# Kernel optimization log

Measured on AMD Instinct MI355X. Metric: run time of the kernel, lower is better.

The kernel has to match this reference:

```python
import jax, jax.numpy as jnp
import numpy as np
from jax import lax

B, C, H, W = 32, 64, 56, 56
G = 4            # num_heads*2 with num_heads=2
SMK, K = 5, 7
C2 = C // 2
HEAD_DIM = C // G
SCALE = HEAD_DIM ** -0.5


def _bias_idx(k, h, w):
    # static replica of ContMix.generate_idx + apply_rpb index construction
    rpb_size = 2 * k - 1
    idx_h = np.arange(k)
    idx_w = np.arange(k)
    idx_k = (idx_h[:, None] * rpb_size + idx_w).reshape(-1)
    rep_h = np.ones(k, np.int64); rep_h[k // 2] = h - (k - 1)
    rep_w = np.ones(k, np.int64); rep_w[k // 2] = w - (k - 1)
    bias_hw = np.repeat(idx_h, rep_h)[:, None] * rpb_size + np.repeat(idx_w, rep_w)  # (h, w)
    bias_idx = (bias_hw[..., None] + idx_k).reshape(-1, k * k)[::-1]  # torch.flip dim 0
    return jnp.asarray(bias_idx.copy())

IDX1 = _bias_idx(SMK, H, W)
IDX2 = _bias_idx(K, H, W)


def setup_inputs() -> dict:
    key = jax.random.key(0)
    ks = jax.random.split(key, 18)
    r = lambda i, sh: jax.random.normal(ks[i], sh, jnp.float32)
    return dict(
        x=r(0, (B, C, H, W)),
        lepe_w=r(1, (C, 1, K, K)) * 0.1,
        lepe_b=r(2, (C,)) * 0.1,
        lepe_bn_s=1.0 + 0.1 * r(3, (C,)),
        lepe_bn_b=0.1 * r(4, (C,)),
        wq_w=r(5, (C2, C2)) * (C2 ** -0.5),
        wq_bn_s=1.0 + 0.1 * r(6, (C2,)),
        wq_bn_b=0.1 * r(7, (C2,)),
        wk_w=r(8, (C2, C2)) * (C2 ** -0.5),
        wk_bn_s=1.0 + 0.1 * r(9, (C2,)),
        wk_bn_b=0.1 * r(10, (C2,)),
        wp_w=r(11, (SMK * SMK + K * K, 49)) * (49 ** -0.5),
        wp_b=0.1 * r(12, (SMK * SMK + K * K,)),
        rpb1=0.02 * r(13, (G, 2 * SMK - 1, 2 * SMK - 1)),
        rpb2=0.02 * r(14, (G, 2 * K - 1, 2 * K - 1)),
        dy_w=r(15, (C, C)) * (C ** -0.5),
        dy_bn_s=1.0 + 0.1 * r(16, (C,)),
        dy_bn_b=0.1 * r(17, (C,)),
    )


def _per_ch(t):
    return t[None, :, None, None]


def _contmix(x, lepe_w, lepe_b, lepe_bn_s, lepe_bn_b, wq_w, wq_bn_s, wq_bn_b,
             wk_w, wk_bn_s, wk_bn_b, wp_w, wp_b, rpb1, rpb2, dy_w, dy_bn_s, dy_bn_b):
    # lepe: deploy-mode DilatedReparamBlock = depthwise 7x7 conv (+bias), then eval BN
    lepe = lax.conv_general_dilated(x, lepe_w, (1, 1), [(K // 2, K // 2)] * 2,
                                    feature_group_count=C)
    lepe = (lepe + _per_ch(lepe_b)) * _per_ch(lepe_bn_s) + _per_ch(lepe_bn_b)

    q, kf = jnp.split(x, 2, axis=1)                         # (B, C2, H, W) each
    q = jnp.einsum('oi,bihw->bohw', wq_w, q)                # weight_query 1x1 conv
    q = (q * _per_ch(wq_bn_s) + _per_ch(wq_bn_b)) * SCALE
    # weight_key: AdaptiveAvgPool2d(7) -> 1x1 conv -> BN (H,W divisible by 7)
    kp = kf.reshape(B, C2, 7, H // 7, 7, W // 7).mean(axis=(3, 5))
    kp = jnp.einsum('oi,bihw->bohw', wk_w, kp)
    kp = kp * _per_ch(wk_bn_s) + _per_ch(wk_bn_b)

    qg = q.reshape(B, G, C2 // G, H * W)                    # b g c n
    kg = kp.reshape(B, G, C2 // G, 49)                      # b g c l
    w = jnp.einsum('bgcn,bgcl->bgnl', qg, kg)               # (B, G, HW, 49)
    # weight_proj: 1x1 conv over the 49 pooled-context channels
    w = jnp.einsum('ml,bgnl->bgnm', wp_w, w) + wp_b         # (B, G, HW, 74)
    w = w.reshape(B, G, H, W, SMK * SMK + K * K)

    attn1 = w[..., :SMK * SMK]
    attn2 = w[..., SMK * SMK:]
    attn1 = attn1 + rpb1.reshape(G, -1)[:, IDX1].reshape(1, G, H, W, SMK * SMK)
    attn2 = attn2 + rpb2.reshape(G, -1)[:, IDX2].reshape(1, G, H, W, K * K)
    attn1 = jax.nn.softmax(attn1, axis=-1)
    attn2 = jax.nn.softmax(attn2, axis=-1)

    c = C // (2 * G)                                        # value head dim = 8
    v = x.reshape(B, 2, G, c, H, W)                         # 'b (m g c) h w'

    def dyn_mix(attn, val, k):
        # unfold + einsum: content-adaptive depthwise mixing
        p = lax.conv_general_dilated_patches(
            val.reshape(B, G * c, H, W), (k, k), (1, 1), [(k // 2, k // 2)] * 2,
            dimension_numbers=('NCHW', 'OIHW', 'NCHW'))
        p = p.reshape(B, G, c, k * k, H, W)                 # channel-major patch layout
        return jnp.einsum('bgckhw,bghwk->bgchw', p, attn)

    x1 = dyn_mix(attn1, v[:, 0], SMK)
    x2 = dyn_mix(attn2, v[:, 1], K)
    out = jnp.concatenate([x1, x2], axis=1).reshape(B, C, H, W)
    out = jnp.einsum('oi,bihw->bohw', dy_w, out)            # dyconv_proj 1x1 + BN
    out = out * _per_ch(dy_bn_s) + _per_ch(dy_bn_b)
    return out + lepe


def reference(x, lepe_w, lepe_b, lepe_bn_s, lepe_bn_b, wq_w, wq_bn_s, wq_bn_b,
              wk_w, wk_bn_s, wk_bn_b, wp_w, wp_b, rpb1, rpb2, dy_w, dy_bn_s, dy_bn_b):
    return _contmix(x, lepe_w, lepe_b, lepe_bn_s, lepe_bn_b, wq_w, wq_bn_s, wq_bn_b,
                    wk_w, wk_bn_s, wk_bn_b, wp_w, wp_b, rpb1, rpb2, dy_w, dy_bn_s, dy_bn_b)
```

## Files before the change

kernel.cpp:

```cpp
#include <hip/hip_runtime.h>

#define BB 32
#define CC 64
#define HH 56
#define WW 56
#define HW 3136
#define TW 64
#define TR 12

__global__ __launch_bounds__(256) void pool_k(const float* __restrict__ x,
                                              float* __restrict__ pws) {
    const int py = blockIdx.x;
    const int b  = blockIdx.y;
    const int tid = threadIdx.x;
    if (tid >= 224) return;
    const int i = tid / 7, px = tid % 7;
    const float4* xp4 = reinterpret_cast<const float4*>(
        x + ((long)(b * CC + 32 + i)) * HW + py * 8 * WW + px * 8);
    float4 sA = make_float4(0.f, 0.f, 0.f, 0.f);
    float4 sB = make_float4(0.f, 0.f, 0.f, 0.f);
    #pragma unroll
    for (int y = 0; y < 8; ++y) {
        const float4 a = xp4[y * 14];
        const float4 c = xp4[y * 14 + 1];
        sA.x += a.x; sA.y += a.y; sA.z += a.z; sA.w += a.w;
        sB.x += c.x; sB.y += c.y; sB.z += c.z; sB.w += c.w;
    }
    pws[(long)b * 1568 + i * 49 + py * 7 + px] =
        (sA.x + sA.y + sA.z + sA.w + sB.x + sB.y + sB.z + sB.w) * (1.f / 64.f);
}

__global__ __launch_bounds__(256) void wk_k(const float* __restrict__ pws,
                                            const float* __restrict__ wk,
                                            const float* __restrict__ wks,
                                            const float* __restrict__ wkb,
                                            const float* __restrict__ wp_w,
                                            float* __restrict__ WK) {
    __shared__ float p_s[32 * 49];
    __shared__ float kg_s[8 * 49];
    const int b = blockIdx.x >> 2;
    const int g = blockIdx.x & 3;
    const int tid = threadIdx.x;
    for (int idx = tid; idx < 1568; idx += 256) p_s[idx] = pws[(long)b * 1568 + idx];
    __syncthreads();
    for (int idx = tid; idx < 392; idx += 256) {
        const int o8 = idx / 49, l = idx % 49;
        const int o = g * 8 + o8;
        float acc = 0.f;
        #pragma unroll
        for (int i = 0; i < 32; ++i) acc = fmaf(wk[o * 32 + i], p_s[i * 49 + l], acc);
        kg_s[idx] = acc * wks[o] + wkb[o];
    }
    __syncthreads();
    for (int idx = tid; idx < 640; idx += 256) {
        const int c = idx / 80, slot = idx % 80;
        float acc = 0.f;
        int m = -1;
        if (slot < 28) { if (slot < 25) m = slot; }
        else           { if (slot < 77) m = 25 + (slot - 28); }
        if (m >= 0) {
            const float* kp = kg_s + c * 49;
            #pragma unroll
            for (int l = 0; l < 49; ++l) acc = fmaf(wp_w[m * 49 + l], kp[l], acc);
        }
        const long base = (long)blockIdx.x * 640;
        if (slot < 28) WK[base + c * 28 + slot] = acc;
        else           WK[base + 224 + c * 52 + (slot - 28)] = acc;
    }
}

__global__ __launch_bounds__(256) void attnmix_k(const float* __restrict__ x,
                                                 const float* __restrict__ WK,
                                                 const float* __restrict__ wq_w,
                                                 const float* __restrict__ wq_s,
                                                 const float* __restrict__ wq_bb,
                                                 const float* __restrict__ wp_b,
                                                 const float* __restrict__ rpb1,
                                                 const float* __restrict__ rpb2,
                                                 const float* __restrict__ lw,
                                                 const float* __restrict__ lb,
                                                 const float* __restrict__ ls,
                                                 const float* __restrict__ lbb,
                                                 float* __restrict__ mix,
                                                 float* __restrict__ out) {
    __shared__ __align__(16) float tile[8 * TR * TW];
    __shared__ __align__(16) float WK1_s[8 * 28];
    __shared__ __align__(16) float WK2_s[8 * 52];
    __shared__ __align__(16) float wqT_s[32 * 8];
    __shared__ __align__(16) float wpb1_s[28];
    __shared__ __align__(16) float wpb2_s[52];
    __shared__ __align__(16) float lw_s[8 * 56];
    __shared__ float rpb1_s[81];
    __shared__ float rpb2_s[169];
    __shared__ float wqbn_s[16];
    __shared__ float lbn_s[48];
    const int tid = threadIdx.x;
    const int bg = blockIdx.y;
    const int g = bg & 3, b = bg >> 2;

    {
        const float* wkp = WK + (long)bg * 640;
        for (int i = tid; i < 224; i += 256) WK1_s[i] = wkp[i];
        for (int i = tid; i < 416; i += 256) WK2_s[i] = wkp[224 + i];
    }
    {
        const int i = tid >> 3, c = tid & 7;
        wqT_s[tid] = wq_w[(g * 8 + c) * 32 + i];
    }
    if (tid < 28) wpb1_s[tid] = (tid < 25) ? wp_b[tid] : 0.f;
    if (tid >= 32 && tid < 84) wpb2_s[tid - 32] = (tid < 81) ? wp_b[25 + tid - 32] : 0.f;
    if (tid < 81) rpb1_s[tid] = rpb1[g * 81 + tid];
    if (tid < 169) rpb2_s[tid] = rpb2[g * 169 + tid];
    if (tid >= 192 && tid < 200) wqbn_s[tid - 192] = wq_s[g * 8 + tid - 192];
    if (tid >= 200 && tid < 208) wqbn_s[8 + tid - 200] = wq_bb[g * 8 + tid - 200];
    for (int i = tid; i < 448; i += 256) {
        const int ch = i / 56, rem = i % 56, row = rem >> 3, j = rem & 7;
        lw_s[i] = (j < 7) ? lw[(g * 8 + ch) * 49 + row * 7 + j] : 0.f;
    }
    if (tid < 16) {
        const int c = (tid < 8) ? (g * 8 + tid) : (32 + g * 8 + tid - 8);
        lbn_s[tid] = lb[c]; lbn_s[16 + tid] = ls[c]; lbn_s[32 + tid] = lbb[c];
    }

    const int N0 = blockIdx.x << 8;
    const int ph0 = N0 / WW;
    const int r0 = ph0 - 3;

    {
        const float* xc = x + ((long)b * CC + g * 8) * HW;
        #pragma unroll
        for (int ch = 0; ch < 8; ++ch)
            for (int k = tid; k < TR * TW; k += 256) {
                const int row = k >> 6, lxx = k & 63;
                const int gy = r0 + row, gx = lxx - 3;
                float v = 0.f;
                if ((unsigned)gy < HH && (unsigned)gx < WW) v = xc[ch * HW + gy * WW + gx];
                tile[ch * (TR * TW) + k] = v;
            }
    }
    __syncthreads();

    const int n = N0 + tid;
    const bool valid = n < HW;
    const int nc = valid ? n : HW - 1;
    const int ph = nc / WW, pw = nc % WW;
    const int yr = HH - 1 - ph, xr = WW - 1 - pw;
    const int lrow = ph - r0;
    const int tb0 = (lrow - 3) * TW + pw;

    const float* xb = x + (long)b * CC * HW + nc;

    float q8[8];
    #pragma unroll
    for (int c = 0; c < 8; ++c) q8[c] = 0.f;
    for (int i = 0; i < 32; ++i) {
        const float xv = xb[i * HW];
        const float4 wA = *reinterpret_cast<const float4*>(wqT_s + i * 8);
        const float4 wB = *reinterpret_cast<const float4*>(wqT_s + i * 8 + 4);
        q8[0] = fmaf(wA.x, xv, q8[0]); q8[1] = fmaf(wA.y, xv, q8[1]);
        q8[2] = fmaf(wA.z, xv, q8[2]); q8[3] = fmaf(wA.w, xv, q8[3]);
        q8[4] = fmaf(wB.x, xv, q8[4]); q8[5] = fmaf(wB.y, xv, q8[5]);
        q8[6] = fmaf(wB.z, xv, q8[6]); q8[7] = fmaf(wB.w, xv, q8[7]);
    }
    #pragma unroll
    for (int c = 0; c < 8; ++c)
        q8[c] = (q8[c] * wqbn_s[c] + wqbn_s[8 + c]) * 0.25f;

    __builtin_amdgcn_sched_barrier(0);

    {
        float w1[25];
        {
            const float4* wp4 = reinterpret_cast<const float4*>(wpb1_s);
            #pragma unroll
            for (int qd = 0; qd < 6; ++qd) {
                const float4 bv = wp4[qd];
                w1[qd * 4 + 0] = bv.x; w1[qd * 4 + 1] = bv.y;
                w1[qd * 4 + 2] = bv.z; w1[qd * 4 + 3] = bv.w;
            }
            w1[24] = wpb1_s[24];
        }
        #pragma unroll
        for (int c = 0; c < 8; ++c) {
            const float qv = q8[c];
            const float4* kr = reinterpret_cast<const float4*>(WK1_s + c * 28);
            #pragma unroll
            for (int qd = 0; qd < 6; ++qd) {
                const float4 kv = kr[qd];
                w1[qd * 4 + 0] = fmaf(qv, kv.x, w1[qd * 4 + 0]);
                w1[qd * 4 + 1] = fmaf(qv, kv.y, w1[qd * 4 + 1]);
                w1[qd * 4 + 2] = fmaf(qv, kv.z, w1[qd * 4 + 2]);
                w1[qd * 4 + 3] = fmaf(qv, kv.w, w1[qd * 4 + 3]);
            }
            w1[24] = fmaf(qv, WK1_s[c * 28 + 24], w1[24]);
        }
        const int rh5 = yr < 2 ? yr : (yr > 53 ? yr - 51 : 2);
        const int rw5 = xr < 2 ? xr : (xr > 53 ? xr - 51 : 2);
        #pragma unroll
        for (int i = 0; i < 5; ++i)
            #pragma unroll
            for (int j = 0; j < 5; ++j)
                w1[i * 5 + j] += rpb1_s[(rh5 + i) * 9 + (rw5 + j)];
        float mx = -1e30f;
        #pragma unroll
        for (int m = 0; m < 25; ++m) mx = fmaxf(mx, w1[m]);
        float sm = 0.f;
        #pragma unroll
        for (int m = 0; m < 25; ++m) { w1[m] = __expf(w1[m] - mx); sm += w1[m]; }
        const float r = 1.f / sm;
        #pragma unroll
        for (int m = 0; m < 25; ++m) w1[m] *= r;

        float* m0 = mix + ((long)b * CC + g * 8) * HW + nc;
        float* o0 = out + ((long)b * CC + g * 8) * HW + nc;
        #pragma unroll
        for (int ch = 0; ch < 8; ++ch) {
            const float* t = tile + ch * (TR * TW) + tb0;
            const float* lwc = lw_s + ch * 56;
            float a = 0.f, la = 0.f;
            #pragma unroll
            for (int i = 0; i < 7; ++i) {
                const float4 lA = *reinterpret_cast<const float4*>(lwc + i * 8);
                const float4 lB = *reinterpret_cast<const float4*>(lwc + i * 8 + 4);
                const float lwv[7] = {lA.x, lA.y, lA.z, lA.w, lB.x, lB.y, lB.z};
                #pragma unroll
                for (int j = 0; j < 7; ++j) {
                    const float v = t[i * TW + j];
                    la = fmaf(lwv[j], v, la);
                    if (i >= 1 && i <= 5 && j >= 1 && j <= 5)
                        a = fmaf(w1[(i - 1) * 5 + (j - 1)], v, a);
                }
            }
            if (valid) {
                m0[ch * HW] = a;
                o0[ch * HW] = (la + lbn_s[ch]) * lbn_s[16 + ch] + lbn_s[32 + ch];
            }
        }
    }

    __syncthreads();
    {
        const float* xc = x + ((long)b * CC + 32 + g * 8) * HW;
        #pragma unroll
        for (int ch = 0; ch < 8; ++ch)
            for (int k = tid; k < TR * TW; k += 256) {
                const int row = k >> 6, lxx = k & 63;
                const int gy = r0 + row, gx = lxx - 3;
                float v = 0.f;
                if ((unsigned)gy < HH && (unsigned)gx < WW) v = xc[ch * HW + gy * WW + gx];
                tile[ch * (TR * TW) + k] = v;
            }
        for (int i = tid; i < 448; i += 256) {
            const int ch = i / 56, rem = i % 56, row = rem >> 3, j = rem & 7;
            lw_s[i] = (j < 7) ? lw[(32 + g * 8 + ch) * 49 + row * 7 + j] : 0.f;
        }
    }
    __syncthreads();

    {
        float w2[49];
        {
            const float4* wp4 = reinterpret_cast<const float4*>(wpb2_s);
            #pragma unroll
            for (int qd = 0; qd < 12; ++qd) {
                const float4 bv = wp4[qd];
                w2[qd * 4 + 0] = bv.x; w2[qd * 4 + 1] = bv.y;
                w2[qd * 4 + 2] = bv.z; w2[qd * 4 + 3] = bv.w;
            }
            w2[48] = wpb2_s[48];
        }
        #pragma unroll
        for (int c = 0; c < 8; ++c) {
            const float qv = q8[c];
            const float4* kr = reinterpret_cast<const float4*>(WK2_s + c * 52);
            #pragma unroll
            for (int qd = 0; qd < 12; ++qd) {
                const float4 kv = kr[qd];
                w2[qd * 4 + 0] = fmaf(qv, kv.x, w2[qd * 4 + 0]);
                w2[qd * 4 + 1] = fmaf(qv, kv.y, w2[qd * 4 + 1]);
                w2[qd * 4 + 2] = fmaf(qv, kv.z, w2[qd * 4 + 2]);
                w2[qd * 4 + 3] = fmaf(qv, kv.w, w2[qd * 4 + 3]);
            }
            w2[48] = fmaf(qv, WK2_s[c * 52 + 48], w2[48]);
        }
        const int rh7 = yr < 3 ? yr : (yr > 52 ? yr - 49 : 3);
        const int rw7 = xr < 3 ? xr : (xr > 52 ? xr - 49 : 3);
        #pragma unroll
        for (int i = 0; i < 7; ++i)
            #pragma unroll
            for (int j = 0; j < 7; ++j)
                w2[i * 7 + j] += rpb2_s[(rh7 + i) * 13 + (rw7 + j)];
        float mx = -1e30f;
        #pragma unroll
        for (int m = 0; m < 49; ++m) mx = fmaxf(mx, w2[m]);
        float sm = 0.f;
        #pragma unroll
        for (int m = 0; m < 49; ++m) { w2[m] = __expf(w2[m] - mx); sm += w2[m]; }
        const float r = 1.f / sm;
        #pragma unroll
        for (int m = 0; m < 49; ++m) w2[m] *= r;

        float* m1 = mix + ((long)b * CC + 32 + g * 8) * HW + nc;
        float* o1 = out + ((long)b * CC + 32 + g * 8) * HW + nc;
        #pragma unroll
        for (int ch = 0; ch < 8; ++ch) {
            const float* t = tile + ch * (TR * TW) + tb0;
            const float* lwc = lw_s + ch * 56;
            float a = 0.f, la = 0.f;
            #pragma unroll
            for (int i = 0; i < 7; ++i) {
                const float4 lA = *reinterpret_cast<const float4*>(lwc + i * 8);
                const float4 lB = *reinterpret_cast<const float4*>(lwc + i * 8 + 4);
                const float lwv[7] = {lA.x, lA.y, lA.z, lA.w, lB.x, lB.y, lB.z};
                #pragma unroll
                for (int j = 0; j < 7; ++j) {
                    const float v = t[i * TW + j];
                    la = fmaf(lwv[j], v, la);
                    a  = fmaf(w2[i * 7 + j], v, a);
                }
            }
            if (valid) {
                m1[ch * HW] = a;
                o1[ch * HW] = (la + lbn_s[8 + ch]) * lbn_s[16 + 8 + ch] + lbn_s[32 + 8 + ch];
            }
        }
    }
}

__global__ __launch_bounds__(256) void final_k(const float* __restrict__ mix,
                                               const float* __restrict__ dy_w,
                                               const float* __restrict__ s,
                                               const float* __restrict__ bb,
                                               float* __restrict__ out) {
    __shared__ float w_s[64 * 64];
    const int tid = threadIdx.x;
    const int b = blockIdx.y;
    for (int i = tid; i < 4096; i += 256) w_s[(i & 63) * 64 + (i >> 6)] = dy_w[i];
    __syncthreads();
    const int oo = (tid >> 5) * 8;
    const int p4 = blockIdx.x * 32 + (tid & 31);
    if (p4 >= 784) return;
    const float* mp = mix + (long)b * CC * HW + p4 * 4;
    float4 acc[8];
    #pragma unroll
    for (int o = 0; o < 8; ++o) acc[o] = make_float4(0.f, 0.f, 0.f, 0.f);
    for (int ii = 0; ii < 64; ii += 8) {
        float4 mv[8];
        #pragma unroll
        for (int u = 0; u < 8; ++u)
            mv[u] = *reinterpret_cast<const float4*>(mp + (long)(ii + u) * HW);
        #pragma unroll
        for (int u = 0; u < 8; ++u) {
            const float* wr = w_s + (ii + u) * 64 + oo;
            #pragma unroll
            for (int o = 0; o < 8; ++o) {
                const float wv = wr[o];
                acc[o].x = fmaf(wv, mv[u].x, acc[o].x);
                acc[o].y = fmaf(wv, mv[u].y, acc[o].y);
                acc[o].z = fmaf(wv, mv[u].z, acc[o].z);
                acc[o].w = fmaf(wv, mv[u].w, acc[o].w);
            }
        }
    }
    float* op = out + (long)b * CC * HW + p4 * 4;
    #pragma unroll
    for (int o = 0; o < 8; ++o) {
        const float sc = s[oo + o], bc = bb[oo + o];
        float4* dst = reinterpret_cast<float4*>(op + (long)(oo + o) * HW);
        float4 prev = *dst;
        prev.x = fmaf(acc[o].x, sc, bc) + prev.x;
        prev.y = fmaf(acc[o].y, sc, bc) + prev.y;
        prev.z = fmaf(acc[o].z, sc, bc) + prev.z;
        prev.w = fmaf(acc[o].w, sc, bc) + prev.w;
        *dst = prev;
    }
}

extern "C" void kernel_launch(void* const* d_in, const int* in_sizes, int n_in,
                              void* d_out, int out_size, void* d_ws, size_t ws_size,
                              hipStream_t stream) {
    const float* x       = (const float*)d_in[0];
    const float* lepe_w  = (const float*)d_in[1];
    const float* lepe_b  = (const float*)d_in[2];
    const float* lepe_s  = (const float*)d_in[3];
    const float* lepe_bb = (const float*)d_in[4];
    const float* wq_w    = (const float*)d_in[5];
    const float* wq_s    = (const float*)d_in[6];
    const float* wq_bb   = (const float*)d_in[7];
    const float* wk_w    = (const float*)d_in[8];
    const float* wk_s    = (const float*)d_in[9];
    const float* wk_bb   = (const float*)d_in[10];
    const float* wp_w    = (const float*)d_in[11];
    const float* wp_b    = (const float*)d_in[12];
    const float* rpb1    = (const float*)d_in[13];
    const float* rpb2    = (const float*)d_in[14];
    const float* dy_w    = (const float*)d_in[15];
    const float* dy_s    = (const float*)d_in[16];
    const float* dy_bb   = (const float*)d_in[17];
    float* out = (float*)d_out;

    float* ws     = (float*)d_ws;
    float* WK_ws  = ws;
    float* mix_ws = WK_ws + 128 * 640;
    float* p_ws   = mix_ws + 32 * 64 * HW;

    const int nTiles = (HW + 255) / 256;

    pool_k<<<dim3(7, BB), 256, 0, stream>>>(x, p_ws);
    wk_k<<<dim3(BB * 4), 256, 0, stream>>>(p_ws, wk_w, wk_s, wk_bb, wp_w, WK_ws);
    attnmix_k<<<dim3(nTiles, BB * 4), 256, 0, stream>>>(x, WK_ws, wq_w, wq_s, wq_bb,
                                                        wp_b, rpb1, rpb2,
                                                        lepe_w, lepe_b, lepe_s, lepe_bb,
                                                        mix_ws, out);
    final_k<<<dim3(25, BB), 256, 0, stream>>>(mix_ws, dy_w, dy_s, dy_bb, out);
}
```

Baseline: 250.3 us.

## Precompute q in separate pass and split attention kernel into two branch kernels

Moves the per-pixel q projection (32→32 1x1 conv with BN and scale) out of the attention kernel into a batched pass that shares a launch with the WK computation, writing q to a workspace buffer. Splits the fused attnmix kernel into attn1 (5x5 branch) and attn2 (7x7 branch), giving each smaller register and shared-memory footprints and twice as many blocks. This is meant to cut the redundant q recompute across the two branches and improve occupancy, at the cost of an extra q write/read through global memory, one more kernel launch, and reloading the x tile in each kernel.

```diff
diff --git a/kernel.cpp b/kernel.cpp
--- a/kernel.cpp
+++ b/kernel.cpp
@@ -30,17 +30,75 @@
         (sA.x + sA.y + sA.z + sA.w + sB.x + sB.y + sB.z + sB.w) * (1.f / 64.f);
 }
 
-__global__ __launch_bounds__(256) void wk_k(const float* __restrict__ pws,
-                                            const float* __restrict__ wk,
-                                            const float* __restrict__ wks,
-                                            const float* __restrict__ wkb,
-                                            const float* __restrict__ wp_w,
-                                            float* __restrict__ WK) {
+__global__ __launch_bounds__(256) void qwk_k(const float* __restrict__ x,
+                                             const float* __restrict__ pws,
+                                             const float* __restrict__ wk,
+                                             const float* __restrict__ wks,
+                                             const float* __restrict__ wkb,
+                                             const float* __restrict__ wp_w,
+                                             const float* __restrict__ wq_w,
+                                             const float* __restrict__ wq_s,
+                                             const float* __restrict__ wq_bb,
+                                             float* __restrict__ WK,
+                                             float* __restrict__ qws) {
     __shared__ float p_s[32 * 49];
     __shared__ float kg_s[8 * 49];
-    const int b = blockIdx.x >> 2;
-    const int g = blockIdx.x & 3;
+    __shared__ float wqT_s[32 * 32];
+    __shared__ float qbn_s[64];
     const int tid = threadIdx.x;
+    const int bx = blockIdx.x;
+
+    if (bx < 800) {
+        for (int idx = tid; idx < 1024; idx += 256) {
+            const int o = idx & 31, i = idx >> 5;
+            wqT_s[i * 32 + o] = wq_w[o * 32 + i];
+        }
+        if (tid < 32) { qbn_s[tid] = wq_s[tid]; qbn_s[32 + tid] = wq_bb[tid]; }
+        __syncthreads();
+        const int b = bx / 25, t = bx % 25;
+        const int p4 = t * 32 + (tid & 31);
+        if (p4 >= 784) return;
+        const int oo = (tid >> 5) * 4;
+        const float* xp = x + (long)b * CC * HW + p4 * 4;
+        float4 acc[4];
+        #pragma unroll
+        for (int o = 0; o < 4; ++o) acc[o] = make_float4(0.f, 0.f, 0.f, 0.f);
+        for (int ii = 0; ii < 32; ii += 8) {
+            float4 mv[8];
+            #pragma unroll
+            for (int u = 0; u < 8; ++u)
+                mv[u] = *reinterpret_cast<const float4*>(xp + (long)(ii + u) * HW);
+            #pragma unroll
+            for (int u = 0; u < 8; ++u) {
+                const float* wr = wqT_s + (ii + u) * 32 + oo;
+                #pragma unroll
+                for (int o = 0; o < 4; ++o) {
+                    const float wv = wr[o];
+                    acc[o].x = fmaf(wv, mv[u].x, acc[o].x);
+                    acc[o].y = fmaf(wv, mv[u].y, acc[o].y);
+                    acc[o].z = fmaf(wv, mv[u].z, acc[o].z);
+                    acc[o].w = fmaf(wv, mv[u].w, acc[o].w);
+                }
+            }
+        }
+        float* qp = qws + (long)b * 32 * HW + p4 * 4;
+        #pragma unroll
+        for (int o = 0; o < 4; ++o) {
+            const float sc = qbn_s[oo + o] * 0.25f;
+            const float bc = qbn_s[32 + oo + o] * 0.25f;
+            float4 r;
+            r.x = fmaf(acc[o].x, sc, bc);
+            r.y = fmaf(acc[o].y, sc, bc);
+            r.z = fmaf(acc[o].z, sc, bc);
+            r.w = fmaf(acc[o].w, sc, bc);
+            *reinterpret_cast<float4*>(qp + (long)(oo + o) * HW) = r;
+        }
+        return;
+    }
+
+    const int id = bx - 800;
+    const int b = id >> 2;
+    const int g = id & 3;
     for (int idx = tid; idx < 1568; idx += 256) p_s[idx] = pws[(long)b * 1568 + idx];
     __syncthreads();
     for (int idx = tid; idx < 392; idx += 256) {
@@ -63,71 +121,68 @@
             #pragma unroll
             for (int l = 0; l < 49; ++l) acc = fmaf(wp_w[m * 49 + l], kp[l], acc);
         }
-        const long base = (long)blockIdx.x * 640;
+        const long base = (long)id * 640;
         if (slot < 28) WK[base + c * 28 + slot] = acc;
         else           WK[base + 224 + c * 52 + (slot - 28)] = acc;
     }
 }
 
-__global__ __launch_bounds__(256) void attnmix_k(const float* __restrict__ x,
-                                                 const float* __restrict__ WK,
-                                                 const float* __restrict__ wq_w,
-                                                 const float* __restrict__ wq_s,
-                                                 const float* __restrict__ wq_bb,
-                                                 const float* __restrict__ wp_b,
-                                                 const float* __restrict__ rpb1,
-                                                 const float* __restrict__ rpb2,
-                                                 const float* __restrict__ lw,
-                                                 const float* __restrict__ lb,
-                                                 const float* __restrict__ ls,
-                                                 const float* __restrict__ lbb,
-                                                 float* __restrict__ mix,
-                                                 float* __restrict__ out) {
+__global__ __launch_bounds__(256) void attn1_k(const float* __restrict__ x,
+                                               const float* __restrict__ WK,
+                                               const float* __restrict__ qws,
+                                               const float* __restrict__ wp_b,
+                                               const float* __restrict__ rpb1,
+                                               const float* __restrict__ lw,
+                                               const float* __restrict__ lb,
+                                               const float* __restrict__ ls,
+                                               const float* __restrict__ lbb,
+                                               float* __restrict__ mix,
+                                               float* __restrict__ out) {
     __shared__ __align__(16) float tile[8 * TR * TW];
     __shared__ __align__(16) float WK1_s[8 * 28];
-    __shared__ __align__(16) float WK2_s[8 * 52];
-    __shared__ __align__(16) float wqT_s[32 * 8];
     __shared__ __align__(16) float wpb1_s[28];
-    __shared__ __align__(16) float wpb2_s[52];
     __shared__ __align__(16) float lw_s[8 * 56];
     __shared__ float rpb1_s[81];
-    __shared__ float rpb2_s[169];
-    __shared__ float wqbn_s[16];
-    __shared__ float lbn_s[48];
+    __shared__ float lbn_s[24];
     const int tid = threadIdx.x;
     const int bg = blockIdx.y;
     const int g = bg & 3, b = bg >> 2;
+    const int ch0 = g * 8;
 
     {
         const float* wkp = WK + (long)bg * 640;
-        for (int i = tid; i < 224; i += 256) WK1_s[i] = wkp[i];
-        for (int i = tid; i < 416; i += 256) WK2_s[i] = wkp[224 + i];
-    }
-    {
-        const int i = tid >> 3, c = tid & 7;
-        wqT_s[tid] = wq_w[(g * 8 + c) * 32 + i];
+        if (tid < 224) WK1_s[tid] = wkp[tid];
     }
     if (tid < 28) wpb1_s[tid] = (tid < 25) ? wp_b[tid] : 0.f;
-    if (tid >= 32 && tid < 84) wpb2_s[tid - 32] = (tid < 81) ? wp_b[25 + tid - 32] : 0.f;
     if (tid < 81) rpb1_s[tid] = rpb1[g * 81 + tid];
-    if (tid < 169) rpb2_s[tid] = rpb2[g * 169 + tid];
-    if (tid >= 192 && tid < 200) wqbn_s[tid - 192] = wq_s[g * 8 + tid - 192];
-    if (tid >= 200 && tid < 208) wqbn_s[8 + tid - 200] = wq_bb[g * 8 + tid - 200];
     for (int i = tid; i < 448; i += 256) {
         const int ch = i / 56, rem = i % 56, row = rem >> 3, j = rem & 7;
-        lw_s[i] = (j < 7) ? lw[(g * 8 + ch) * 49 + row * 7 + j] : 0.f;
-    }
-    if (tid < 16) {
-        const int c = (tid < 8) ? (g * 8 + tid) : (32 + g * 8 + tid - 8);
-        lbn_s[tid] = lb[c]; lbn_s[16 + tid] = ls[c]; lbn_s[32 + tid] = lbb[c];
+        lw_s[i] = (j < 7) ? lw[(ch0 + ch) * 49 + row * 7 + j] : 0.f;
+    }
+    if (tid >= 232 && tid < 240) {
+        const int c = ch0 + tid - 232;
+        lbn_s[tid - 232] = lb[c]; lbn_s[8 + tid - 232] = ls[c]; lbn_s[16 + tid - 232] = lbb[c];
     }
 
     const int N0 = blockIdx.x << 8;
     const int ph0 = N0 / WW;
     const int r0 = ph0 - 3;
 
-    {
-        const float* xc = x + ((long)b * CC + g * 8) * HW;
+    const int n = N0 + tid;
+    const bool valid = n < HW;
+    const int nc = valid ? n : HW - 1;
+    const int ph = nc / WW, pw = nc % WW;
+    const int yr = HH - 1 - ph, xr = WW - 1 - pw;
+    const int lrow = ph - r0;
+    const int tb0 = (lrow - 3) * TW + pw;
+
+    const float* qp = qws + ((long)b * 32 + ch0) * HW + nc;
+    float q8[8];
+    #pragma unroll
+    for (int c = 0; c < 8; ++c) q8[c] = qp[c * HW];
+
+    {
+        const float* xc = x + ((long)b * CC + ch0) * HW;
         #pragma unroll
         for (int ch = 0; ch < 8; ++ch)
             for (int k = tid; k < TR * TW; k += 256) {
@@ -140,6 +195,116 @@
     }
     __syncthreads();
 
+    float w1[25];
+    {
+        const float4* wp4 = reinterpret_cast<const float4*>(wpb1_s);
+        #pragma unroll
+        for (int qd = 0; qd < 6; ++qd) {
+            const float4 bv = wp4[qd];
+            w1[qd * 4 + 0] = bv.x; w1[qd * 4 + 1] = bv.y;
+            w1[qd * 4 + 2] = bv.z; w1[qd * 4 + 3] = bv.w;
+        }
+        w1[24] = wpb1_s[24];
+    }
+    #pragma unroll
+    for (int c = 0; c < 8; ++c) {
+        const float qv = q8[c];
+        const float4* kr = reinterpret_cast<const float4*>(WK1_s + c * 28);
+        #pragma unroll
+        for (int qd = 0; qd < 6; ++qd) {
+            const float4 kv = kr[qd];
+            w1[qd * 4 + 0] = fmaf(qv, kv.x, w1[qd * 4 + 0]);
+            w1[qd * 4 + 1] = fmaf(qv, kv.y, w1[qd * 4 + 1]);
+            w1[qd * 4 + 2] = fmaf(qv, kv.z, w1[qd * 4 + 2]);
+            w1[qd * 4 + 3] = fmaf(qv, kv.w, w1[qd * 4 + 3]);
+        }
+        w1[24] = fmaf(qv, WK1_s[c * 28 + 24], w1[24]);
+    }
+    const int rh5 = yr < 2 ? yr : (yr > 53 ? yr - 51 : 2);
+    const int rw5 = xr < 2 ? xr : (xr > 53 ? xr - 51 : 2);
+    #pragma unroll
+    for (int i = 0; i < 5; ++i)
+        #pragma unroll
+        for (int j = 0; j < 5; ++j)
+            w1[i * 5 + j] += rpb1_s[(rh5 + i) * 9 + (rw5 + j)];
+    float mx = -1e30f;
+    #pragma unroll
+    for (int m = 0; m < 25; ++m) mx = fmaxf(mx, w1[m]);
+    float sm = 0.f;
+    #pragma unroll
+    for (int m = 0; m < 25; ++m) { w1[m] = __expf(w1[m] - mx); sm += w1[m]; }
+    const float r = 1.f / sm;
+    #pragma unroll
+    for (int m = 0; m < 25; ++m) w1[m] *= r;
+
+    float* m0 = mix + ((long)b * CC + ch0) * HW + nc;
+    float* o0 = out + ((long)b * CC + ch0) * HW + nc;
+    #pragma unroll
+    for (int ch = 0; ch < 8; ++ch) {
+        const float* t = tile + ch * (TR * TW) + tb0;
+        const float* lwc = lw_s + ch * 56;
+        float a = 0.f, la = 0.f;
+        #pragma unroll
+        for (int i = 0; i < 7; ++i) {
+            const float4 lA = *reinterpret_cast<const float4*>(lwc + i * 8);
+            const float4 lB = *reinterpret_cast<const float4*>(lwc + i * 8 + 4);
+            const float lwv[7] = {lA.x, lA.y, lA.z, lA.w, lB.x, lB.y, lB.z};
+            #pragma unroll
+            for (int j = 0; j < 7; ++j) {
+                const float v = t[i * TW + j];
+                la = fmaf(lwv[j], v, la);
+                if (i >= 1 && i <= 5 && j >= 1 && j <= 5)
+                    a = fmaf(w1[(i - 1) * 5 + (j - 1)], v, a);
+            }
+        }
+        if (valid) {
+            m0[ch * HW] = a;
+            o0[ch * HW] = (la + lbn_s[ch]) * lbn_s[8 + ch] + lbn_s[16 + ch];
+        }
+    }
+}
+
+__global__ __launch_bounds__(256) void attn2_k(const float* __restrict__ x,
+                                               const float* __restrict__ WK,
+                                               const float* __restrict__ qws,
+                                               const float* __restrict__ wp_b,
+                                               const float* __restrict__ rpb2,
+                                               const float* __restrict__ lw,
+                                               const float* __restrict__ lb,
+                                               const float* __restrict__ ls,
+                                               const float* __restrict__ lbb,
+                                               float* __restrict__ mix,
+                                               float* __restrict__ out) {
+    __shared__ __align__(16) float tile[8 * TR * TW];
+    __shared__ __align__(16) float WK2_s[8 * 52];
+    __shared__ __align__(16) float wpb2_s[52];
+    __shared__ __align__(16) float lw_s[8 * 56];
+    __shared__ float rpb2_s[169];
+    __shared__ float lbn_s[24];
+    const int tid = threadIdx.x;
+    const int bg = blockIdx.y;
+    const int g = bg & 3, b = bg >> 2;
+    const int ch0 = 32 + g * 8;
+
+    {
+        const float* wkp = WK + (long)bg * 640 + 224;
+        for (int i = tid; i < 416; i += 256) WK2_s[i] = wkp[i];
+    }
+    if (tid < 52) wpb2_s[tid] = (tid < 49) ? wp_b[25 + tid] : 0.f;
+    if (tid >= 64 && tid < 233) rpb2_s[tid - 64] = rpb2[g * 169 + (tid - 64)];
+    for (int i = tid; i < 448; i += 256) {
+        const int ch = i / 56, rem = i % 56, row = rem >> 3, j = rem & 7;
+        lw_s[i] = (j < 7) ? lw[(ch0 + ch) * 49 + row * 7 + j] : 0.f;
+    }
+    if (tid >= 240 && tid < 248) {
+        const int c = ch0 + tid - 240;
+        lbn_s[tid - 240] = lb[c]; lbn_s[8 + tid - 240] = ls[c]; lbn_s[16 + tid - 240] = lbb[c];
+    }
+
+    const int N0 = blockIdx.x << 8;
+    const int ph0 = N0 / WW;
+    const int r0 = ph0 - 3;
+
     const int n = N0 + tid;
     const bool valid = n < HW;
     const int nc = valid ? n : HW - 1;
@@ -148,99 +313,13 @@
     const int lrow = ph - r0;
     const int tb0 = (lrow - 3) * TW + pw;
 
-    const float* xb = x + (long)b * CC * HW + nc;
-
+    const float* qp = qws + ((long)b * 32 + g * 8) * HW + nc;
     float q8[8];
     #pragma unroll
-    for (int c = 0; c < 8; ++c) q8[c] = 0.f;
-    for (int i = 0; i < 32; ++i) {
-        const float xv = xb[i * HW];
-        const float4 wA = *reinterpret_cast<const float4*>(wqT_s + i * 8);
-        const float4 wB = *reinterpret_cast<const float4*>(wqT_s + i * 8 + 4);
-        q8[0] = fmaf(wA.x, xv, q8[0]); q8[1] = fmaf(wA.y, xv, q8[1]);
-        q8[2] = fmaf(wA.z, xv, q8[2]); q8[3] = fmaf(wA.w, xv, q8[3]);
-        q8[4] = fmaf(wB.x, xv, q8[4]); q8[5] = fmaf(wB.y, xv, q8[5]);
-        q8[6] = fmaf(wB.z, xv, q8[6]); q8[7] = fmaf(wB.w, xv, q8[7]);
-    }
-    #pragma unroll
-    for (int c = 0; c < 8; ++c)
-        q8[c] = (q8[c] * wqbn_s[c] + wqbn_s[8 + c]) * 0.25f;
-
-    __builtin_amdgcn_sched_barrier(0);
-
-    {
-        float w1[25];
-        {
-            const float4* wp4 = reinterpret_cast<const float4*>(wpb1_s);
-            #pragma unroll
-            for (int qd = 0; qd < 6; ++qd) {
-                const float4 bv = wp4[qd];
-                w1[qd * 4 + 0] = bv.x; w1[qd * 4 + 1] = bv.y;
-                w1[qd * 4 + 2] = bv.z; w1[qd * 4 + 3] = bv.w;
-            }
-            w1[24] = wpb1_s[24];
-        }
-        #pragma unroll
-        for (int c = 0; c < 8; ++c) {
-            const float qv = q8[c];
-            const float4* kr = reinterpret_cast<const float4*>(WK1_s + c * 28);
-            #pragma unroll
-            for (int qd = 0; qd < 6; ++qd) {
-                const float4 kv = kr[qd];
-                w1[qd * 4 + 0] = fmaf(qv, kv.x, w1[qd * 4 + 0]);
-                w1[qd * 4 + 1] = fmaf(qv, kv.y, w1[qd * 4 + 1]);
-                w1[qd * 4 + 2] = fmaf(qv, kv.z, w1[qd * 4 + 2]);
-                w1[qd * 4 + 3] = fmaf(qv, kv.w, w1[qd * 4 + 3]);
-            }
-            w1[24] = fmaf(qv, WK1_s[c * 28 + 24], w1[24]);
-        }
-        const int rh5 = yr < 2 ? yr : (yr > 53 ? yr - 51 : 2);
-        const int rw5 = xr < 2 ? xr : (xr > 53 ? xr - 51 : 2);
-        #pragma unroll
-        for (int i = 0; i < 5; ++i)
-            #pragma unroll
-            for (int j = 0; j < 5; ++j)
-                w1[i * 5 + j] += rpb1_s[(rh5 + i) * 9 + (rw5 + j)];
-        float mx = -1e30f;
-        #pragma unroll
-        for (int m = 0; m < 25; ++m) mx = fmaxf(mx, w1[m]);
-        float sm = 0.f;
-        #pragma unroll
-        for (int m = 0; m < 25; ++m) { w1[m] = __expf(w1[m] - mx); sm += w1[m]; }
-        const float r = 1.f / sm;
-        #pragma unroll
-        for (int m = 0; m < 25; ++m) w1[m] *= r;
-
-        float* m0 = mix + ((long)b * CC + g * 8) * HW + nc;
-        float* o0 = out + ((long)b * CC + g * 8) * HW + nc;
-        #pragma unroll
-        for (int ch = 0; ch < 8; ++ch) {
-            const float* t = tile + ch * (TR * TW) + tb0;
-            const float* lwc = lw_s + ch * 56;
-            float a = 0.f, la = 0.f;
-            #pragma unroll
-            for (int i = 0; i < 7; ++i) {
-                const float4 lA = *reinterpret_cast<const float4*>(lwc + i * 8);
-                const float4 lB = *reinterpret_cast<const float4*>(lwc + i * 8 + 4);
-                const float lwv[7] = {lA.x, lA.y, lA.z, lA.w, lB.x, lB.y, lB.z};
-                #pragma unroll
-                for (int j = 0; j < 7; ++j) {
-                    const float v = t[i * TW + j];
-                    la = fmaf(lwv[j], v, la);
-                    if (i >= 1 && i <= 5 && j >= 1 && j <= 5)
-                        a = fmaf(w1[(i - 1) * 5 + (j - 1)], v, a);
-                }
-            }
-            if (valid) {
-                m0[ch * HW] = a;
-                o0[ch * HW] = (la + lbn_s[ch]) * lbn_s[16 + ch] + lbn_s[32 + ch];
-            }
-        }
-    }
-
-    __syncthreads();
-    {
-        const float* xc = x + ((long)b * CC + 32 + g * 8) * HW;
+    for (int c = 0; c < 8; ++c) q8[c] = qp[c * HW];
+
+    {
+        const float* xc = x + ((long)b * CC + ch0) * HW;
         #pragma unroll
         for (int ch = 0; ch < 8; ++ch)
             for (int k = tid; k < TR * TW; k += 256) {
@@ -250,79 +329,73 @@
                 if ((unsigned)gy < HH && (unsigned)gx < WW) v = xc[ch * HW + gy * WW + gx];
                 tile[ch * (TR * TW) + k] = v;
             }
-        for (int i = tid; i < 448; i += 256) {
-            const int ch = i / 56, rem = i % 56, row = rem >> 3, j = rem & 7;
-            lw_s[i] = (j < 7) ? lw[(32 + g * 8 + ch) * 49 + row * 7 + j] : 0.f;
-        }
     }
     __syncthreads();
 
-    {
-        float w2[49];
-        {
-            const float4* wp4 = reinterpret_cast<const float4*>(wpb2_s);
-            #pragma unroll
-            for (int qd = 0; qd < 12; ++qd) {
-                const float4 bv = wp4[qd];
-                w2[qd * 4 + 0] = bv.x; w2[qd * 4 + 1] = bv.y;
-                w2[qd * 4 + 2] = bv.z; w2[qd * 4 + 3] = bv.w;
-            }
-            w2[48] = wpb2_s[48];
-        }
-        #pragma unroll
-        for (int c = 0; c < 8; ++c) {
-            const float qv = q8[c];
-            const float4* kr = reinterpret_cast<const float4*>(WK2_s + c * 52);
-            #pragma unroll
-            for (int qd = 0; qd < 12; ++qd) {
-                const float4 kv = kr[qd];
-                w2[qd * 4 + 0] = fmaf(qv, kv.x, w2[qd * 4 + 0]);
-                w2[qd * 4 + 1] = fmaf(qv, kv.y, w2[qd * 4 + 1]);
-                w2[qd * 4 + 2] = fmaf(qv, kv.z, w2[qd * 4 + 2]);
-                w2[qd * 4 + 3] = fmaf(qv, kv.w, w2[qd * 4 + 3]);
-            }
-            w2[48] = fmaf(qv, WK2_s[c * 52 + 48], w2[48]);
-        }
-        const int rh7 = yr < 3 ? yr : (yr > 52 ? yr - 49 : 3);
-        const int rw7 = xr < 3 ? xr : (xr > 52 ? xr - 49 : 3);
-        #pragma unroll
-        for (int i = 0; i < 7; ++i)
-            #pragma unroll
-            for (int j = 0; j < 7; ++j)
-                w2[i * 7 + j] += rpb2_s[(rh7 + i) * 13 + (rw7 + j)];
-        float mx = -1e30f;
-        #pragma unroll
-        for (int m = 0; m < 49; ++m) mx = fmaxf(mx, w2[m]);
-        float sm = 0.f;
-        #pragma unroll
-        for (int m = 0; m < 49; ++m) { w2[m] = __expf(w2[m] - mx); sm += w2[m]; }
-        const float r = 1.f / sm;
-        #pragma unroll
-        for (int m = 0; m < 49; ++m) w2[m] *= r;
-
-        float* m1 = mix + ((long)b * CC + 32 + g * 8) * HW + nc;
-        float* o1 = out + ((long)b * CC + 32 + g * 8) * HW + nc;
-        #pragma unroll
-        for (int ch = 0; ch < 8; ++ch) {
-            const float* t = tile + ch * (TR * TW) + tb0;
-            const float* lwc = lw_s + ch * 56;
-            float a = 0.f, la = 0.f;
-            #pragma unroll
-            for (int i = 0; i < 7; ++i) {
-                const float4 lA = *reinterpret_cast<const float4*>(lwc + i * 8);
-                const float4 lB = *reinterpret_cast<const float4*>(lwc + i * 8 + 4);
-                const float lwv[7] = {lA.x, lA.y, lA.z, lA.w, lB.x, lB.y, lB.z};
-                #pragma unroll
-                for (int j = 0; j < 7; ++j) {
-                    const float v = t[i * TW + j];
-                    la = fmaf(lwv[j], v, la);
-                    a  = fmaf(w2[i * 7 + j], v, a);
-                }
-            }
-            if (valid) {
-                m1[ch * HW] = a;
-                o1[ch * HW] = (la + lbn_s[8 + ch]) * lbn_s[16 + 8 + ch] + lbn_s[32 + 8 + ch];
-            }
+    float w2[49];
+    {
+        const float4* wp4 = reinterpret_cast<const float4*>(wpb2_s);
+        #pragma unroll
+        for (int qd = 0; qd < 12; ++qd) {
+            const float4 bv = wp4[qd];
+            w2[qd * 4 + 0] = bv.x; w2[qd * 4 + 1] = bv.y;
+            w2[qd * 4 + 2] = bv.z; w2[qd * 4 + 3] = bv.w;
+        }
+        w2[48] = wpb2_s[48];
+    }
+    #pragma unroll
+    for (int c = 0; c < 8; ++c) {
+        const float qv = q8[c];
+        const float4* kr = reinterpret_cast<const float4*>(WK2_s + c * 52);
+        #pragma unroll
+        for (int qd = 0; qd < 12; ++qd) {
+            const float4 kv = kr[qd];
+            w2[qd * 4 + 0] = fmaf(qv, kv.x, w2[qd * 4 + 0]);
+            w2[qd * 4 + 1] = fmaf(qv, kv.y, w2[qd * 4 + 1]);
+            w2[qd * 4 + 2] = fmaf(qv, kv.z, w2[qd * 4 + 2]);
+            w2[qd * 4 + 3] = fmaf(qv, kv.w, w2[qd * 4 + 3]);
+        }
+        w2[48] = fmaf(qv, WK2_s[c * 52 + 48], w2[48]);
+    }
+    const int rh7 = yr < 3 ? yr : (yr > 52 ? yr - 49 : 3);
+    const int rw7 = xr < 3 ? xr : (xr > 52 ? xr - 49 : 3);
+    #pragma unroll
+    for (int i = 0; i < 7; ++i)
+        #pragma unroll
+        for (int j = 0; j < 7; ++j)
+            w2[i * 7 + j] += rpb2_s[(rh7 + i) * 13 + (rw7 + j)];
+    float mx = -1e30f;
+    #pragma unroll
+    for (int m = 0; m < 49; ++m) mx = fmaxf(mx, w2[m]);
+    float sm = 0.f;
+    #pragma unroll
+    for (int m = 0; m < 49; ++m) { w2[m] = __expf(w2[m] - mx); sm += w2[m]; }
+    const float r = 1.f / sm;
+    #pragma unroll
+    for (int m = 0; m < 49; ++m) w2[m] *= r;
+
+    float* m1 = mix + ((long)b * CC + ch0) * HW + nc;
+    float* o1 = out + ((long)b * CC + ch0) * HW + nc;
+    #pragma unroll
+    for (int ch = 0; ch < 8; ++ch) {
+        const float* t = tile + ch * (TR * TW) + tb0;
+        const float* lwc = lw_s + ch * 56;
+        float a = 0.f, la = 0.f;
+        #pragma unroll
+        for (int i = 0; i < 7; ++i) {
+            const float4 lA = *reinterpret_cast<const float4*>(lwc + i * 8);
+            const float4 lB = *reinterpret_cast<const float4*>(lwc + i * 8 + 4);
+            const float lwv[7] = {lA.x, lA.y, lA.z, lA.w, lB.x, lB.y, lB.z};
+            #pragma unroll
+            for (int j = 0; j < 7; ++j) {
+                const float v = t[i * TW + j];
+                la = fmaf(lwv[j], v, la);
+                a  = fmaf(w2[i * 7 + j], v, a);
+            }
+        }
+        if (valid) {
+            m1[ch * HW] = a;
+            o1[ch * HW] = (la + lbn_s[ch]) * lbn_s[8 + ch] + lbn_s[16 + ch];
         }
     }
 }
@@ -403,14 +476,18 @@
     float* WK_ws  = ws;
     float* mix_ws = WK_ws + 128 * 640;
     float* p_ws   = mix_ws + 32 * 64 * HW;
+    float* q_ws   = p_ws + 32 * 1568;
 
     const int nTiles = (HW + 255) / 256;
 
     pool_k<<<dim3(7, BB), 256, 0, stream>>>(x, p_ws);
-    wk_k<<<dim3(BB * 4), 256, 0, stream>>>(p_ws, wk_w, wk_s, wk_bb, wp_w, WK_ws);
-    attnmix_k<<<dim3(nTiles, BB * 4), 256, 0, stream>>>(x, WK_ws, wq_w, wq_s, wq_bb,
-                                                        wp_b, rpb1, rpb2,
-                                                        lepe_w, lepe_b, lepe_s, lepe_bb,
-                                                        mix_ws, out);
+    qwk_k<<<dim3(800 + BB * 4), 256, 0, stream>>>(x, p_ws, wk_w, wk_s, wk_bb, wp_w,
+                                                  wq_w, wq_s, wq_bb, WK_ws, q_ws);
+    attn1_k<<<dim3(nTiles, BB * 4), 256, 0, stream>>>(x, WK_ws, q_ws, wp_b, rpb1,
+                                                      lepe_w, lepe_b, lepe_s, lepe_bb,
+                                                      mix_ws, out);
+    attn2_k<<<dim3(nTiles, BB * 4), 256, 0, stream>>>(x, WK_ws, q_ws, wp_b, rpb2,
+                                                      lepe_w, lepe_b, lepe_s, lepe_bb,
+                                                      mix_ws, out);
     final_k<<<dim3(25, BB), 256, 0, stream>>>(mix_ws, dy_w, dy_s, dy_bb, out);
 }
```

New measurement: 257.1 us. 1.03x slower.

## Split attnmix channels across two thread halves with 512-thread blocks

Applied to the files above, without the earlier changes.

Doubles the attnmix block to 512 threads. Each pixel is now handled by two threads, and each thread mixes 4 of the 8 channels, which halves the per-thread stencil work and raises parallelism. The cost is duplicated work: both halves recompute the q projection and both softmaxes for the same pixel. Register pressure under launch bounds of 512 may also force spills, and the sched_barrier is removed.

```diff
diff --git a/kernel.cpp b/kernel.cpp
--- a/kernel.cpp
+++ b/kernel.cpp
@@ -69,7 +69,7 @@
     }
 }
 
-__global__ __launch_bounds__(256) void attnmix_k(const float* __restrict__ x,
+__global__ __launch_bounds__(512) void attnmix_k(const float* __restrict__ x,
                                                  const float* __restrict__ WK,
                                                  const float* __restrict__ wq_w,
                                                  const float* __restrict__ wq_s,
@@ -95,31 +95,34 @@
     __shared__ float wqbn_s[16];
     __shared__ float lbn_s[48];
     const int tid = threadIdx.x;
+    const int px = tid & 255;
+    const int cb = (tid >> 8) * 4;
     const int bg = blockIdx.y;
     const int g = bg & 3, b = bg >> 2;
 
     {
         const float* wkp = WK + (long)bg * 640;
-        for (int i = tid; i < 224; i += 256) WK1_s[i] = wkp[i];
-        for (int i = tid; i < 416; i += 256) WK2_s[i] = wkp[224 + i];
-    }
-    {
+        for (int i = tid; i < 224; i += 512) WK1_s[i] = wkp[i];
+        for (int i = tid; i < 416; i += 512) WK2_s[i] = wkp[224 + i];
+    }
+    if (tid < 256) {
         const int i = tid >> 3, c = tid & 7;
         wqT_s[tid] = wq_w[(g * 8 + c) * 32 + i];
     }
-    if (tid < 28) wpb1_s[tid] = (tid < 25) ? wp_b[tid] : 0.f;
-    if (tid >= 32 && tid < 84) wpb2_s[tid - 32] = (tid < 81) ? wp_b[25 + tid - 32] : 0.f;
-    if (tid < 81) rpb1_s[tid] = rpb1[g * 81 + tid];
-    if (tid < 169) rpb2_s[tid] = rpb2[g * 169 + tid];
-    if (tid >= 192 && tid < 200) wqbn_s[tid - 192] = wq_s[g * 8 + tid - 192];
-    if (tid >= 200 && tid < 208) wqbn_s[8 + tid - 200] = wq_bb[g * 8 + tid - 200];
-    for (int i = tid; i < 448; i += 256) {
-        const int ch = i / 56, rem = i % 56, row = rem >> 3, j = rem & 7;
-        lw_s[i] = (j < 7) ? lw[(g * 8 + ch) * 49 + row * 7 + j] : 0.f;
-    }
-    if (tid < 16) {
-        const int c = (tid < 8) ? (g * 8 + tid) : (32 + g * 8 + tid - 8);
-        lbn_s[tid] = lb[c]; lbn_s[16 + tid] = ls[c]; lbn_s[32 + tid] = lbb[c];
+    if (tid >= 256 && tid < 284) wpb1_s[tid - 256] = (tid < 281) ? wp_b[tid - 256] : 0.f;
+    if (tid >= 288 && tid < 340) wpb2_s[tid - 288] = (tid < 337) ? wp_b[25 + tid - 288] : 0.f;
+    if (tid >= 340 && tid < 421) rpb1_s[tid - 340] = rpb1[g * 81 + (tid - 340)];
+    if (tid >= 343 && tid < 512) rpb2_s[tid - 343] = rpb2[g * 169 + (tid - 343)];
+    if (tid >= 320 && tid < 328) wqbn_s[tid - 320] = wq_s[g * 8 + tid - 320];
+    if (tid >= 328 && tid < 336) wqbn_s[8 + tid - 328] = wq_bb[g * 8 + tid - 328];
+    if (tid < 448) {
+        const int ch = tid / 56, rem = tid % 56, row = rem >> 3, j = rem & 7;
+        lw_s[tid] = (j < 7) ? lw[(g * 8 + ch) * 49 + row * 7 + j] : 0.f;
+    }
+    if (tid >= 464 && tid < 480) {
+        const int t16 = tid - 464;
+        const int c = (t16 < 8) ? (g * 8 + t16) : (32 + g * 8 + t16 - 8);
+        lbn_s[t16] = lb[c]; lbn_s[16 + t16] = ls[c]; lbn_s[32 + t16] = lbb[c];
     }
 
     const int N0 = blockIdx.x << 8;
@@ -128,19 +131,18 @@
 
     {
         const float* xc = x + ((long)b * CC + g * 8) * HW;
-        #pragma unroll
-        for (int ch = 0; ch < 8; ++ch)
-            for (int k = tid; k < TR * TW; k += 256) {
-                const int row = k >> 6, lxx = k & 63;
-                const int gy = r0 + row, gx = lxx - 3;
-                float v = 0.f;
-                if ((unsigned)gy < HH && (unsigned)gx < WW) v = xc[ch * HW + gy * WW + gx];
-                tile[ch * (TR * TW) + k] = v;
-            }
-    }
-    __syncthreads();
-
-    const int n = N0 + tid;
+        for (int idx = tid; idx < 8 * TR * TW; idx += 512) {
+            const int ch = idx / (TR * TW), k = idx % (TR * TW);
+            const int row = k >> 6, lxx = k & 63;
+            const int gy = r0 + row, gx = lxx - 3;
+            float v = 0.f;
+            if ((unsigned)gy < HH && (unsigned)gx < WW) v = xc[ch * HW + gy * WW + gx];
+            tile[idx] = v;
+        }
+    }
+    __syncthreads();
+
+    const int n = N0 + px;
     const bool valid = n < HW;
     const int nc = valid ? n : HW - 1;
     const int ph = nc / WW, pw = nc % WW;
@@ -166,8 +168,6 @@
     for (int c = 0; c < 8; ++c)
         q8[c] = (q8[c] * wqbn_s[c] + wqbn_s[8 + c]) * 0.25f;
 
-    __builtin_amdgcn_sched_barrier(0);
-
     {
         float w1[25];
         {
@@ -211,12 +211,12 @@
         #pragma unroll
         for (int m = 0; m < 25; ++m) w1[m] *= r;
 
-        float* m0 = mix + ((long)b * CC + g * 8) * HW + nc;
-        float* o0 = out + ((long)b * CC + g * 8) * HW + nc;
-        #pragma unroll
-        for (int ch = 0; ch < 8; ++ch) {
-            const float* t = tile + ch * (TR * TW) + tb0;
-            const float* lwc = lw_s + ch * 56;
+        float* m0 = mix + ((long)b * CC + g * 8 + cb) * HW + nc;
+        float* o0 = out + ((long)b * CC + g * 8 + cb) * HW + nc;
+        #pragma unroll
+        for (int ch = 0; ch < 4; ++ch) {
+            const float* t = tile + (cb + ch) * (TR * TW) + tb0;
+            const float* lwc = lw_s + (cb + ch) * 56;
             float a = 0.f, la = 0.f;
             #pragma unroll
             for (int i = 0; i < 7; ++i) {
@@ -233,7 +233,7 @@
             }
             if (valid) {
                 m0[ch * HW] = a;
-                o0[ch * HW] = (la + lbn_s[ch]) * lbn_s[16 + ch] + lbn_s[32 + ch];
+                o0[ch * HW] = (la + lbn_s[cb + ch]) * lbn_s[16 + cb + ch] + lbn_s[32 + cb + ch];
             }
         }
     }
@@ -241,18 +241,17 @@
     __syncthreads();
     {
         const float* xc = x + ((long)b * CC + 32 + g * 8) * HW;
-        #pragma unroll
-        for (int ch = 0; ch < 8; ++ch)
-            for (int k = tid; k < TR * TW; k += 256) {
-                const int row = k >> 6, lxx = k & 63;
-                const int gy = r0 + row, gx = lxx - 3;
-                float v = 0.f;
-                if ((unsigned)gy < HH && (unsigned)gx < WW) v = xc[ch * HW + gy * WW + gx];
-                tile[ch * (TR * TW) + k] = v;
-            }
-        for (int i = tid; i < 448; i += 256) {
-            const int ch = i / 56, rem = i % 56, row = rem >> 3, j = rem & 7;
-            lw_s[i] = (j < 7) ? lw[(32 + g * 8 + ch) * 49 + row * 7 + j] : 0.f;
+        for (int idx = tid; idx < 8 * TR * TW; idx += 512) {
+            const int ch = idx / (TR * TW), k = idx % (TR * TW);
+            const int row = k >> 6, lxx = k & 63;
+            const int gy = r0 + row, gx = lxx - 3;
+            float v = 0.f;
+            if ((unsigned)gy < HH && (unsigned)gx < WW) v = xc[ch * HW + gy * WW + gx];
+            tile[idx] = v;
+        }
+        if (tid < 448) {
+            const int ch = tid / 56, rem = tid % 56, row = rem >> 3, j = rem & 7;
+            lw_s[tid] = (j < 7) ? lw[(32 + g * 8 + ch) * 49 + row * 7 + j] : 0.f;
         }
     }
     __syncthreads();
@@ -300,12 +299,12 @@
         #pragma unroll
         for (int m = 0; m < 49; ++m) w2[m] *= r;
 
-        float* m1 = mix + ((long)b * CC + 32 + g * 8) * HW + nc;
-        float* o1 = out + ((long)b * CC + 32 + g * 8) * HW + nc;
-        #pragma unroll
-        for (int ch = 0; ch < 8; ++ch) {
-            const float* t = tile + ch * (TR * TW) + tb0;
-            const float* lwc = lw_s + ch * 56;
+        float* m1 = mix + ((long)b * CC + 32 + g * 8 + cb) * HW + nc;
+        float* o1 = out + ((long)b * CC + 32 + g * 8 + cb) * HW + nc;
+        #pragma unroll
+        for (int ch = 0; ch < 4; ++ch) {
+            const float* t = tile + (cb + ch) * (TR * TW) + tb0;
+            const float* lwc = lw_s + (cb + ch) * 56;
             float a = 0.f, la = 0.f;
             #pragma unroll
             for (int i = 0; i < 7; ++i) {
@@ -321,7 +320,7 @@
             }
             if (valid) {
                 m1[ch * HW] = a;
-                o1[ch * HW] = (la + lbn_s[8 + ch]) * lbn_s[16 + 8 + ch] + lbn_s[32 + 8 + ch];
+                o1[ch * HW] = (la + lbn_s[8 + cb + ch]) * lbn_s[16 + 8 + cb + ch] + lbn_s[32 + 8 + cb + ch];
             }
         }
     }
@@ -408,7 +407,7 @@
 
     pool_k<<<dim3(7, BB), 256, 0, stream>>>(x, p_ws);
     wk_k<<<dim3(BB * 4), 256, 0, stream>>>(p_ws, wk_w, wk_s, wk_bb, wp_w, WK_ws);
-    attnmix_k<<<dim3(nTiles, BB * 4), 256, 0, stream>>>(x, WK_ws, wq_w, wq_s, wq_bb,
+    attnmix_k<<<dim3(nTiles, BB * 4), 512, 0, stream>>>(x, WK_ws, wq_w, wq_s, wq_bb,
                                                         wp_b, rpb1, rpb2,
                                                         lepe_w, lepe_b, lepe_s, lepe_bb,
                                                         mix_ws, out);
```

After: 295.4 us. 1.18x slower.
